# Kernel tuning notes

Measured on AMD Instinct MI355X. Metric: run time of the kernel, lower is better.

The kernel has to match this reference:

```python
import jax, jax.numpy as jnp
import numpy as np

H, DH = 12, 64
EPS = 1e-6
ROPE_BASE = 100.0

def rms_norm(x, scale=None, eps=EPS):
    xf = x.astype(jnp.float32)
    n = xf * jax.lax.rsqrt(jnp.mean(xf * xf, axis=-1, keepdims=True) + eps)
    if scale is not None:
        n = n * scale.astype(jnp.float32)
    return n.astype(x.dtype)

def rotate_half(x):
    h = x.shape[-1] // 2
    return jnp.concatenate([-x[..., h:], x[..., :h]], axis=-1)

def rope_cos_sin(pos_ids, head_dim, base=ROPE_BASE):
    # pos_ids: [B, N, 2] int -> cos/sin [B, N, head_dim]
    dim = head_dim // 2
    inv = 1.0 / base ** (jnp.arange(0, dim, 2, dtype=jnp.float32) / dim)  # [dim//2]
    cos_l, sin_l = [], []
    for i in range(2):  # x and y coordinate
        pos = pos_ids[:, :, i].astype(jnp.float32)           # [B, N]
        freqs = pos[:, :, None] * inv[None, None, :]          # [B, N, dim//2]
        emb = jnp.concatenate([freqs, freqs], axis=-1)        # [B, N, dim]
        cos_l.append(jnp.cos(emb))
        sin_l.append(jnp.sin(emb))
    return jnp.concatenate(cos_l, axis=-1), jnp.concatenate(sin_l, axis=-1)

def apply_2d_rope(x, cos, sin):
    # x: [B, N, H, Dh]; cos/sin: [B, N, Dh]; split channels evenly between x/y.
    c = x.shape[-1] // 2
    outs = []
    for k in range(2):
        xs = x[..., k * c:(k + 1) * c]
        cc = cos[:, :, None, k * c:(k + 1) * c]
        ss = sin[:, :, None, k * c:(k + 1) * c]
        outs.append(xs * cc + rotate_half(xs) * ss)
    return jnp.concatenate(outs, axis=-1)

def setup_inputs() -> dict:
    key = jax.random.key(0)
    ks = jax.random.split(key, 7)
    B, N, D = 8, 1024, 768
    hidden_states = jax.random.normal(ks[0], (B, N, D), dtype=jnp.float32)
    pixel_position_ids = jax.random.randint(ks[1], (B, N, 2), 0, 32, dtype=jnp.int32)
    s = 0.02
    Wq = jax.random.normal(ks[2], (H * DH, D), dtype=jnp.float32) * s
    Wk = jax.random.normal(ks[3], (H * DH, D), dtype=jnp.float32) * s
    Wv = jax.random.normal(ks[4], (H * DH, D), dtype=jnp.float32) * s
    Wo = jax.random.normal(ks[5], (D, H * DH), dtype=jnp.float32) * s
    q_scale = jnp.ones((DH,), dtype=jnp.float32)
    k_scale = jnp.ones((DH,), dtype=jnp.float32)
    return {"hidden_states": hidden_states, "pixel_position_ids": pixel_position_ids,
            "Wq": Wq, "Wk": Wk, "Wv": Wv, "Wo": Wo,
            "q_scale": q_scale, "k_scale": k_scale}

def reference(hidden_states, pixel_position_ids, Wq, Wk, Wv, Wo, q_scale, k_scale):
    B, N, D = hidden_states.shape
    # QKV projections (clip bounds are +/-inf -> no-op). Weights are [out, in].
    q = (hidden_states @ Wq.T).reshape(B, N, H, DH)
    k = (hidden_states @ Wk.T).reshape(B, N, H, DH)
    v = (hidden_states @ Wv.T).reshape(B, N, H, DH)
    # Per-head RMSNorm (v has no learned scale)
    q = rms_norm(q, q_scale)
    k = rms_norm(k, k_scale)
    v = rms_norm(v, None)
    # 2D RoPE
    cos, sin = rope_cos_sin(pixel_position_ids, DH)
    q = apply_2d_rope(q, cos, sin)
    k = apply_2d_rope(k, cos, sin)
    # Full attention, scaling = 1.0, softmax in fp32
    scores = jnp.einsum('bqhd,bkhd->bhqk', q, k)
    attn = jax.nn.softmax(scores.astype(jnp.float32), axis=-1).astype(q.dtype)
    out = jnp.einsum('bhqk,bkhd->bqhd', attn, v).reshape(B, N, H * DH)
    return out @ Wo.T
```

## Files before the change

kernel.cpp:

```cpp
#include <hip/hip_runtime.h>

typedef _Float16 f16;
typedef __attribute__((ext_vector_type(8))) _Float16 f16x8;
typedef __attribute__((ext_vector_type(4))) _Float16 f16x4;
typedef __attribute__((ext_vector_type(2))) __fp16 h16x2;
typedef __attribute__((ext_vector_type(4))) float f32x4;

#define NH 12
#define DHD 64
#define NB 8
#define NSEQ 1024
#define DMODEL 768
#define BHN (NB*NH)
#define ROWS_PER (BHN*NSEQ)

#define MFMA(a,b,c) __builtin_amdgcn_mfma_f32_16x16x32_f16(a,b,c,0,0,0)

__device__ __forceinline__ void gload16(const void* g, void* l) {
  __builtin_amdgcn_global_load_lds(
      (__attribute__((address_space(1))) void*)(g),
      (__attribute__((address_space(3))) void*)(l), 16, 0, 0);
}

__global__ __launch_bounds__(256) void cast_kernel(const float* __restrict__ in,
                                                   f16* __restrict__ out, int n) {
  int i = (blockIdx.x * blockDim.x + threadIdx.x) * 4;
  if (i < n) {
    float4 v = *(const float4*)(in + i);
    f16x4 o = {(f16)v.x, (f16)v.y, (f16)v.z, (f16)v.w};
    *(f16x4*)(out + i) = o;
  }
}

__global__ __launch_bounds__(256) void cast_w_kernel(const float* __restrict__ Wq,
                                                     const float* __restrict__ Wk,
                                                     const float* __restrict__ Wv,
                                                     const float* __restrict__ Wo,
                                                     f16* __restrict__ Wf,
                                                     f16* __restrict__ Wof,
                                                     float2* __restrict__ rtab, int nw) {
  int i = (blockIdx.x * blockDim.x + threadIdx.x) * 4;
  if (i < 4*nw) {
    int which = i / nw;
    int off = i - which*nw;
    const float* src = (which == 0) ? Wq : (which == 1) ? Wk : (which == 2) ? Wv : Wo;
    f16* dst = (which < 3) ? (Wf + (size_t)which*nw + off) : (Wof + off);
    float4 v = *(const float4*)(src + off);
    f16x4 o = {(f16)v.x, (f16)v.y, (f16)v.z, (f16)v.w};
    *(f16x4*)dst = o;
  }
  if (blockIdx.x == 0) {
    for (int e = threadIdx.x; e < 512; e += 256) {
      int pos = e >> 4, k = e & 15;
      float ang = (float)pos * __expf((float)k * (-4.605170185988091f / 16.0f));
      float sn, cs;
      __sincosf(ang, &sn, &cs);
      rtab[e] = make_float2(cs, sn);
    }
  }
}

template<int MODE>
__global__ __launch_bounds__(512) void gemm_bt(const f16* __restrict__ A,
                                               const f16* __restrict__ B,
                                               float* __restrict__ Cout,
                                               f16* __restrict__ QKout,
                                               f16* __restrict__ Vout,
                                               const int* __restrict__ pos_ids,
                                               const float* __restrict__ q_scale,
                                               const float* __restrict__ k_scale,
                                               const float2* __restrict__ rtab,
                                               int M, int N, int K) {
  constexpr int BN = (MODE == 1) ? 128 : 64;
  constexpr int NJ = BN / 32;
  constexpr int ABUF = 8192;
  constexpr int BBUF = BN*64;
  __shared__ __align__(16) f16 SH[2*ABUF + 2*BBUF];
  const int tid = threadIdx.x;
  const int w = tid >> 6, l = tid & 63;
  const int wr = w >> 1, wc = w & 1;
  const int g = l >> 4, i16 = l & 15;

  int bx, by;
  {
    int id = blockIdx.x;
    const int nbx = (MODE == 1) ? 18 : 12;
    const int chunk = (MODE == 1) ? 144 : 96;
    int idp = (id & 7) * chunk + (id >> 3);
    by = idp / nbx; bx = idp - by * nbx;
  }

  const f32x4 fzero = {0.f, 0.f, 0.f, 0.f};
  f32x4 acc[2][NJ];
#pragma unroll
  for (int i = 0; i < 2; i++)
#pragma unroll
    for (int j = 0; j < NJ; j++) acc[i][j] = fzero;

  const int srow = tid >> 3;
  const int schunk = (tid & 7) ^ (srow & 7);
  const size_t arow = (size_t)(by*128 + srow)*K + schunk*8;
  const size_t brow = (size_t)(bx*BN + srow)*K + schunk*8;

  const int nt = K / 64;
#define STAGE(buf, k0)                                                          \
  {                                                                             \
    char* AlB = (char*)(SH + (buf)*ABUF) + w*1024;                              \
    char* BlB = (char*)(SH + 2*ABUF + (buf)*BBUF) + w*1024;                     \
    _Pragma("unroll")                                                           \
    for (int n = 0; n < 2; ++n)                                                 \
      gload16(A + arow + (size_t)(n*64)*K + (k0), AlB + n*8192);                \
    _Pragma("unroll")                                                           \
    for (int n = 0; n < BN/64; ++n)                                             \
      gload16(B + brow + (size_t)(n*64)*K + (k0), BlB + n*8192);                \
  }

  STAGE(0, 0);
  __syncthreads();
  for (int t = 0; t < nt; ++t) {
    const int buf = t & 1;
    if (t + 1 < nt) STAGE(buf ^ 1, (t + 1)*64);
    const f16* Ac = SH + buf*ABUF;
    const f16* Bc = SH + 2*ABUF + buf*BBUF;
#pragma unroll
    for (int kk = 0; kk < 2; ++kk) {
      f16x8 af[2], bfr[NJ];
#pragma unroll
      for (int i = 0; i < 2; i++)
        af[i] = *(const f16x8*)(Ac + (wr*32 + i*16 + i16)*64 + ((kk*4 + g) ^ (i16 & 7))*8);
#pragma unroll
      for (int j = 0; j < NJ; j++)
        bfr[j] = *(const f16x8*)(Bc + (wc*(BN/2) + j*16 + i16)*64 + ((kk*4 + g) ^ (i16 & 7))*8);
#pragma unroll
      for (int i = 0; i < 2; i++)
#pragma unroll
        for (int j = 0; j < NJ; j++)
          acc[i][j] = MFMA(af[i], bfr[j], acc[i][j]);
    }
    __syncthreads();
  }
#undef STAGE

  const int m0 = by*128 + wr*32;
  const int n0 = bx*BN + wc*(BN/2);
  if constexpr (MODE == 0) {
#pragma unroll
    for (int i = 0; i < 2; i++)
#pragma unroll
      for (int j = 0; j < NJ; j++)
#pragma unroll
        for (int r = 0; r < 4; r++) {
          int m = m0 + i*16 + g*4 + r;
          int n = n0 + j*16 + i16;
          Cout[(size_t)m*N + n] = acc[i][j][r];
        }
  } else {
  if (bx >= 12) {
    const int h0 = (bx - 12)*2;
    const int bb = by >> 3;
    const int ns0 = (by & 7) * 128;
    f16* Lt = SH;
#pragma unroll
    for (int i = 0; i < 2; i++) {
      f32x4 ssv = fzero;
#pragma unroll
      for (int j = 0; j < 4; j++)
#pragma unroll
        for (int r = 0; r < 4; r++) ssv[r] += acc[i][j][r]*acc[i][j][r];
#pragma unroll
      for (int d = 1; d < 16; d <<= 1)
#pragma unroll
        for (int r = 0; r < 4; r++) ssv[r] += __shfl_xor(ssv[r], d);
#pragma unroll
      for (int r = 0; r < 4; r++) {
        float rinv = rsqrtf(ssv[r] * (1.0f/64.0f) + 1e-6f);
        int nsl = wr*32 + i*16 + g*4 + r;
#pragma unroll
        for (int j = 0; j < 4; j++)
          Lt[(wc*64 + j*16 + i16)*136 + nsl] = (f16)(acc[i][j][r]*rinv);
      }
    }
    __syncthreads();
    const int dh = tid >> 2, q4 = tid & 3;
    f16* dst = Vout + ((size_t)((bb*NH + h0 + (dh >> 6))*64 + (dh & 63)))*1024
               + ns0 + q4*32;
    const f16* ls = Lt + dh*136 + q4*32;
#pragma unroll
    for (int e = 0; e < 4; ++e)
      *(uint4*)(dst + e*8) = *(const uint4*)(ls + e*8);
  } else {
    const int qkv = n0 / DMODEL;
    const int h = (n0 - qkv*DMODEL) >> 6;
    const float* scp = (qkv == 0) ? q_scale : k_scale;
    float scl[4];
#pragma unroll
    for (int j = 0; j < 4; j++) {
      scl[j] = scp[j*16 + i16];
      if (qkv == 0) scl[j] *= 1.4426950408889634f;
    }
    const float2* rt = rtab + i16;
#pragma unroll
    for (int i = 0; i < 2; i++) {
      f32x4 ssv = fzero;
#pragma unroll
      for (int j = 0; j < 4; j++)
#pragma unroll
        for (int r = 0; r < 4; r++) ssv[r] += acc[i][j][r]*acc[i][j][r];
#pragma unroll
      for (int d = 1; d < 16; d <<= 1)
#pragma unroll
        for (int r = 0; r < 4; r++) ssv[r] += __shfl_xor(ssv[r], d);
#pragma unroll
      for (int r = 0; r < 4; r++) {
        int m = m0 + i*16 + g*4 + r;
        int bb = m >> 10, ns = m & 1023;
        float rinv = rsqrtf(ssv[r] * (1.0f/64.0f) + 1e-6f);
        int2 pp = *(const int2*)(pos_ids + ((size_t)bb*NSEQ + ns)*2);
        float2 t0 = rt[pp.x*16];
        float2 t1 = rt[pp.y*16];
        float x0 = acc[i][0][r]*rinv*scl[0];
        float x1 = acc[i][1][r]*rinv*scl[1];
        float x2 = acc[i][2][r]*rinv*scl[2];
        float x3 = acc[i][3][r]*rinv*scl[3];
        size_t row = ((size_t)qkv*BHN + bb*NH + h)*NSEQ + ns;
        f16* ob = QKout + row*64;
        ob[i16]      = (f16)(x0*t0.x - x1*t0.y);
        ob[16 + i16] = (f16)(x1*t0.x + x0*t0.y);
        ob[32 + i16] = (f16)(x2*t1.x - x3*t1.y);
        ob[48 + i16] = (f16)(x3*t1.x + x2*t1.y);
      }
    }
  }
  }
}

__device__ __forceinline__ int sigma_perm(int p) {
  return (p & 0x20) | ((p & 0xC) << 1) | ((p & 0x10) >> 2) | (p & 3);
}

#define FM3(a,b,c) fmaxf(fmaxf(a,b),c)

__global__ __launch_bounds__(512) void attn_kernel(const f16* __restrict__ QKu,
                                                   const f16* __restrict__ Vtu,
                                                   f16* __restrict__ O) {
  const int id = blockIdx.x;
  const int xcd = id & 7, idx = id >> 3;
  const int bh = xcd*12 + (idx >> 3);
  const int q0 = (idx & 7) * 128;
  const int tid = threadIdx.x, w = tid >> 6, l = tid & 63;
  const int g = l >> 4, i16 = l & 15;
  const int g4 = g*4;
  const int sw = i16 & 7;
  const int b = bh / NH, h = bh - b*NH;

  __shared__ __align__(16) f16 Ks[2*64*64];
  __shared__ __align__(16) f16 Vs[2*64*64];

  const f16* qrow = QKu + ((size_t)bh*NSEQ + q0 + w*16 + i16)*64;
  f16x8 q0f = *(const f16x8*)(qrow + g*8);
  f16x8 q1f = *(const f16x8*)(qrow + 32 + g*8);

  const char* Kb  = (const char*)(QKu + (size_t)(BHN + bh)*NSEQ*64);
  const char* Vtb = (const char*)(Vtu + (size_t)bh*64*1024);
  const int prow0 = w*8 + (l >> 3);
  const int cl = (l & 7) ^ (l >> 3);
  const char* Ksrc = Kb + sigma_perm(prow0)*128 + cl*16;
  const char* Vsrc = Vtb + prow0*2048 + cl*16;

  const f32x4 fzero = {0.f, 0.f, 0.f, 0.f};
  const f16x8 vones = {(f16)1.f,(f16)1.f,(f16)1.f,(f16)1.f,
                       (f16)1.f,(f16)1.f,(f16)1.f,(f16)1.f};
  float mR = -1e30f;
  f32x4 o[4];
  f32x4 acc_l = fzero;
#pragma unroll
  for (int t = 0; t < 4; t++) o[t] = fzero;

  int cur = 0;
  {
    gload16(Ksrc, (char*)Ks + w*1024);
    gload16(Vsrc, (char*)Vs + w*1024);
  }
  __syncthreads();

  for (int t = 0; t < 16; ++t) {
    if (t < 15) {
      gload16(Ksrc + (t+1)*8192, (char*)Ks + (cur^1)*8192 + w*1024);
      gload16(Vsrc + (t+1)*128,  (char*)Vs + (cur^1)*8192 + w*1024);
    }
    const f16* Kc = Ks + cur*4096;
    const f16* Vc = Vs + cur*4096;

    f32x4 s[4] = {fzero, fzero, fzero, fzero};
    __builtin_amdgcn_s_setprio(1);
#pragma unroll
    for (int j = 0; j < 4; ++j) {
      const f16* kr = Kc + (j*16 + i16)*64;
      f16x8 k0 = *(const f16x8*)(kr + (g ^ sw)*8);
      f16x8 k1 = *(const f16x8*)(kr + ((g^4) ^ sw)*8);
      s[j] = MFMA(k0, q0f, s[j]);
      s[j] = MFMA(k1, q1f, s[j]);
    }
    __builtin_amdgcn_s_setprio(0);

    float t0m = FM3(s[0][0], s[0][1], s[0][2]);
    float t1m = FM3(s[0][3], s[1][0], s[1][1]);
    float t2m = FM3(s[1][2], s[1][3], s[2][0]);
    float t3m = FM3(s[2][1], s[2][2], s[2][3]);
    float t4m = FM3(s[3][0], s[3][1], s[3][2]);
    float tm = fmaxf(FM3(FM3(t0m, t1m, t2m), t3m, t4m), s[3][3]);
    tm = fmaxf(tm, __shfl_xor(tm, 16));
    tm = fmaxf(tm, __shfl_xor(tm, 32));
    if (__any(tm > mR + 11.5416f)) {
      float nm = fmaxf(mR, tm);
      float fac = __builtin_amdgcn_exp2f(mR - nm);
      mR = nm;
#pragma unroll
      for (int r = 0; r < 4; ++r) {
        float fr = __shfl(fac, g4 + r);
        o[0][r] *= fr; o[1][r] *= fr; o[2][r] *= fr; o[3][r] *= fr;
        acc_l[r] *= fr;
      }
    }
#pragma unroll
    for (int j = 0; j < 4; ++j)
#pragma unroll
      for (int r = 0; r < 4; ++r) s[j][r] = __builtin_amdgcn_exp2f(s[j][r] - mR);

    union { h16x2 h[4]; f16x8 v; } u0, u1;
    u0.h[0] = __builtin_amdgcn_cvt_pkrtz(s[0][0], s[0][1]);
    u0.h[1] = __builtin_amdgcn_cvt_pkrtz(s[0][2], s[0][3]);
    u0.h[2] = __builtin_amdgcn_cvt_pkrtz(s[1][0], s[1][1]);
    u0.h[3] = __builtin_amdgcn_cvt_pkrtz(s[1][2], s[1][3]);
    u1.h[0] = __builtin_amdgcn_cvt_pkrtz(s[2][0], s[2][1]);
    u1.h[1] = __builtin_amdgcn_cvt_pkrtz(s[2][2], s[2][3]);
    u1.h[2] = __builtin_amdgcn_cvt_pkrtz(s[3][0], s[3][1]);
    u1.h[3] = __builtin_amdgcn_cvt_pkrtz(s[3][2], s[3][3]);
    f16x8 pa0 = u0.v, pa1 = u1.v;

    __builtin_amdgcn_s_setprio(1);
#pragma unroll
    for (int t2 = 0; t2 < 4; ++t2) {
      const f16* vr = Vc + (t2*16 + i16)*64;
      f16x8 bv0 = *(const f16x8*)(vr + (g ^ sw)*8);
      f16x8 bv1 = *(const f16x8*)(vr + ((g^4) ^ sw)*8);
      o[t2] = MFMA(pa0, bv0, o[t2]);
      o[t2] = MFMA(pa1, bv1, o[t2]);
    }
    acc_l = MFMA(pa0, vones, acc_l);
    acc_l = MFMA(pa1, vones, acc_l);
    __builtin_amdgcn_s_setprio(0);

    __syncthreads();
    cur ^= 1;
  }

#pragma unroll
  for (int r = 0; r < 4; ++r) {
    float invl = 1.0f / acc_l[r];
    int q = q0 + w*16 + g4 + r;
    size_t base = ((size_t)(b*NSEQ + q))*DMODEL + h*DHD;
#pragma unroll
    for (int t2 = 0; t2 < 4; ++t2)
      O[base + t2*16 + i16] = (f16)(o[t2][r] * invl);
  }
}

extern "C" void kernel_launch(void* const* d_in, const int* in_sizes, int n_in,
                              void* d_out, int out_size, void* d_ws, size_t ws_size,
                              hipStream_t stream) {
  const float* hs = (const float*)d_in[0];
  const int*   pos = (const int*)d_in[1];
  const float* Wq = (const float*)d_in[2];
  const float* Wk = (const float*)d_in[3];
  const float* Wv = (const float*)d_in[4];
  const float* Wo = (const float*)d_in[5];
  const float* qs = (const float*)d_in[6];
  const float* ks = (const float*)d_in[7];

  const int nhs = 8192*768;
  const int nw  = 768*768;

  char* p = (char*)d_ws;
  f16* Xf   = (f16*)p; p += (size_t)nhs*2;
  f16* Wf   = (f16*)p; p += (size_t)3*nw*2;
  f16* Wof  = (f16*)p; p += (size_t)nw*2;
  f16* QKpk = (f16*)p; p += (size_t)2*ROWS_PER*64*2;
  f16* Vt   = (f16*)p; p += (size_t)ROWS_PER*64*2;
  f16* Ob   = (f16*)p; p += (size_t)nhs*2;
  float2* Rtab = (float2*)p; p += 512*sizeof(float2);

  cast_kernel<<<nhs/1024, 256, 0, stream>>>(hs, Xf, nhs);
  cast_w_kernel<<<(4*nw)/1024, 256, 0, stream>>>(Wq, Wk, Wv, Wo, Wf, Wof, Rtab, nw);

  gemm_bt<1><<<1152, 512, 0, stream>>>(Xf, Wf, nullptr, QKpk, Vt,
                                       pos, qs, ks, Rtab, 8192, 2304, 768);
  attn_kernel<<<768, 512, 0, stream>>>(QKpk, Vt, Ob);
  gemm_bt<0><<<768, 512, 0, stream>>>(Ob, Wof, (float*)d_out, nullptr, nullptr,
                                      nullptr, nullptr, nullptr, nullptr, 8192, 768, 768);
}
```

Measured before the change: 112.4 us.

## Split K across wave pairs in GEMM with LDS reduction of partial accumulators

Restructures the GEMM wave layout so each pair of waves splits the 64-wide K step: each wave computes a 64xBN/2 tile over half of K. This cuts LDS fragment reads per MFMA because each A fragment is reused across more B fragments. Partial accumulators are then exchanged and reduced through LDS, with extra barriers in the epilogue, and each wave keeps half the rows. The cost is doubled accumulator registers, which may hurt occupancy, and the launch bound now also requests a minimum block count.

```diff
diff --git a/kernel.cpp b/kernel.cpp
--- a/kernel.cpp
+++ b/kernel.cpp
@@ -61,7 +61,7 @@
 }
 
 template<int MODE>
-__global__ __launch_bounds__(512) void gemm_bt(const f16* __restrict__ A,
+__global__ __launch_bounds__(512, 4) void gemm_bt(const f16* __restrict__ A,
                                                const f16* __restrict__ B,
                                                float* __restrict__ Cout,
                                                f16* __restrict__ QKout,
@@ -78,7 +78,9 @@
   __shared__ __align__(16) f16 SH[2*ABUF + 2*BBUF];
   const int tid = threadIdx.x;
   const int w = tid >> 6, l = tid & 63;
-  const int wr = w >> 1, wc = w & 1;
+  const int wq = w & 1;
+  const int ws = w >> 1;
+  const int wr = ws >> 1, wc = ws & 1;
   const int g = l >> 4, i16 = l & 15;
 
   int bx, by;
@@ -91,9 +93,9 @@
   }
 
   const f32x4 fzero = {0.f, 0.f, 0.f, 0.f};
-  f32x4 acc[2][NJ];
-#pragma unroll
-  for (int i = 0; i < 2; i++)
+  f32x4 acc[4][NJ];
+#pragma unroll
+  for (int i = 0; i < 4; i++)
 #pragma unroll
     for (int j = 0; j < NJ; j++) acc[i][j] = fzero;
 
@@ -122,30 +124,62 @@
     if (t + 1 < nt) STAGE(buf ^ 1, (t + 1)*64);
     const f16* Ac = SH + buf*ABUF;
     const f16* Bc = SH + 2*ABUF + buf*BBUF;
-#pragma unroll
-    for (int kk = 0; kk < 2; ++kk) {
-      f16x8 af[2], bfr[NJ];
-#pragma unroll
-      for (int i = 0; i < 2; i++)
-        af[i] = *(const f16x8*)(Ac + (wr*32 + i*16 + i16)*64 + ((kk*4 + g) ^ (i16 & 7))*8);
+    f16x8 af[4], bfr[NJ];
+#pragma unroll
+    for (int i = 0; i < 4; i++)
+      af[i] = *(const f16x8*)(Ac + (wr*64 + i*16 + i16)*64 + ((wq*4 + g) ^ (i16 & 7))*8);
+#pragma unroll
+    for (int j = 0; j < NJ; j++)
+      bfr[j] = *(const f16x8*)(Bc + (wc*(BN/2) + j*16 + i16)*64 + ((wq*4 + g) ^ (i16 & 7))*8);
+#pragma unroll
+    for (int i = 0; i < 4; i++)
 #pragma unroll
       for (int j = 0; j < NJ; j++)
-        bfr[j] = *(const f16x8*)(Bc + (wc*(BN/2) + j*16 + i16)*64 + ((kk*4 + g) ^ (i16 & 7))*8);
-#pragma unroll
-      for (int i = 0; i < 2; i++)
-#pragma unroll
-        for (int j = 0; j < NJ; j++)
-          acc[i][j] = MFMA(af[i], bfr[j], acc[i][j]);
-    }
+        acc[i][j] = MFMA(af[i], bfr[j], acc[i][j]);
     __syncthreads();
   }
 #undef STAGE
 
-  const int m0 = by*128 + wr*32;
+  {
+    float* Xch = (float*)SH;
+    const int xw = ws*(2*NJ*256) + l*4;
+    if (wq) {
+#pragma unroll
+      for (int il = 0; il < 2; ++il)
+#pragma unroll
+        for (int j = 0; j < NJ; ++j)
+          *(f32x4*)(Xch + xw + (il*NJ + j)*256) = acc[il][j];
+    }
+    __syncthreads();
+    if (!wq) {
+#pragma unroll
+      for (int il = 0; il < 2; ++il)
+#pragma unroll
+        for (int j = 0; j < NJ; ++j)
+          acc[il][j] += *(const f32x4*)(Xch + xw + (il*NJ + j)*256);
+#pragma unroll
+      for (int il = 0; il < 2; ++il)
+#pragma unroll
+        for (int j = 0; j < NJ; ++j)
+          *(f32x4*)(Xch + xw + (il*NJ + j)*256) = acc[2 + il][j];
+    }
+    __syncthreads();
+    if (wq) {
+#pragma unroll
+      for (int il = 0; il < 2; ++il)
+#pragma unroll
+        for (int j = 0; j < NJ; ++j)
+          acc[2 + il][j] += *(const f32x4*)(Xch + xw + (il*NJ + j)*256);
+    }
+    __syncthreads();
+  }
+
+  const int m0 = by*128 + wr*64;
   const int n0 = bx*BN + wc*(BN/2);
   if constexpr (MODE == 0) {
 #pragma unroll
-    for (int i = 0; i < 2; i++)
+    for (int il = 0; il < 2; ++il) {
+      const int i = wq*2 + il;
 #pragma unroll
       for (int j = 0; j < NJ; j++)
 #pragma unroll
@@ -154,6 +188,7 @@
           int n = n0 + j*16 + i16;
           Cout[(size_t)m*N + n] = acc[i][j][r];
         }
+    }
   } else {
   if (bx >= 12) {
     const int h0 = (bx - 12)*2;
@@ -161,7 +196,8 @@
     const int ns0 = (by & 7) * 128;
     f16* Lt = SH;
 #pragma unroll
-    for (int i = 0; i < 2; i++) {
+    for (int il = 0; il < 2; ++il) {
+      const int i = wq*2 + il;
       f32x4 ssv = fzero;
 #pragma unroll
       for (int j = 0; j < 4; j++)
@@ -174,7 +210,7 @@
 #pragma unroll
       for (int r = 0; r < 4; r++) {
         float rinv = rsqrtf(ssv[r] * (1.0f/64.0f) + 1e-6f);
-        int nsl = wr*32 + i*16 + g*4 + r;
+        int nsl = wr*64 + i*16 + g*4 + r;
 #pragma unroll
         for (int j = 0; j < 4; j++)
           Lt[(wc*64 + j*16 + i16)*136 + nsl] = (f16)(acc[i][j][r]*rinv);
@@ -200,7 +236,8 @@
     }
     const float2* rt = rtab + i16;
 #pragma unroll
-    for (int i = 0; i < 2; i++) {
+    for (int il = 0; il < 2; ++il) {
+      const int i = wq*2 + il;
       f32x4 ssv = fzero;
 #pragma unroll
       for (int j = 0; j < 4; j++)
```

Result: slower. 405.7 us (+260.9%).
